# Optimization experiments

Hardware: AMD Instinct MI355X
Metric: run time of the kernel (lower is better)

The kernel has to match this reference:

```python
import jax, jax.numpy as jnp
import numpy as np

B, N, L, H, N_NODE, STEP = 512, 50, 50, 128, 100000, 1


def setup_inputs() -> dict:
    key = jax.random.key(0)
    ks = jax.random.split(key, 24)
    stdv = 1.0 / np.sqrt(H)
    u = lambda k, shape: jax.random.uniform(k, shape, jnp.float32, -stdv, stdv)
    inp = {
        "items": jax.random.randint(ks[0], (B, N), 0, N_NODE),
        "A": jax.random.uniform(ks[1], (B, N, 2 * N), jnp.float32),
        "alias_inputs": jax.random.randint(ks[2], (B, L), 0, N),
        "embedding": u(ks[3], (N_NODE, H)),
        "w_ih": u(ks[4], (3 * H, 2 * H)),
        "w_hh": u(ks[5], (3 * H, H)),
        "b_ih": u(ks[6], (3 * H,)),
        "b_hh": u(ks[7], (3 * H,)),
        "b_iah": u(ks[8], (H,)),
        "b_oah": u(ks[9], (H,)),
        "W_ein": u(ks[10], (H, H)), "b_ein": u(ks[11], (H,)),
        "W_eout": u(ks[12], (H, H)), "b_eout": u(ks[13], (H,)),
        "W1": u(ks[14], (H, H)), "b1": u(ks[15], (H,)),
        "W2": u(ks[16], (H, H)), "b2": u(ks[17], (H,)),
        "W3": u(ks[18], (1, H)),
        "Wt": u(ks[19], (H, 2 * H)), "bt": u(ks[20], (H,)),
    }
    return inp


def reference(items, A, alias_inputs, embedding, w_ih, w_hh, b_ih, b_hh,
              b_iah, b_oah, W_ein, b_ein, W_eout, b_eout,
              W1, b1, W2, b2, W3, Wt, bt):
    hidden = embedding[items]  # [B,N,H]
    A_in, A_out = A[:, :, :N], A[:, :, N:2 * N]
    for _ in range(STEP):
        # GRU-style GNN cell
        h_in = jnp.matmul(A_in, hidden @ W_ein.T + b_ein) + b_iah   # [B,N,H]
        h_out = jnp.matmul(A_out, hidden @ W_eout.T + b_eout) + b_oah
        inputs = jnp.concatenate([h_in, h_out], axis=2)             # [B,N,2H]
        gi = inputs @ w_ih.T + b_ih                                  # [B,N,3H]
        gh = hidden @ w_hh.T + b_hh
        i_r, i_i, i_n = jnp.split(gi, 3, axis=2)
        h_r, h_i, h_n = jnp.split(gh, 3, axis=2)
        resetgate = jax.nn.sigmoid(i_r + h_r)
        inputgate = jax.nn.sigmoid(i_i + h_i)
        newgate = jnp.tanh(i_n + resetgate * h_n)
        hidden = newgate + inputgate * (hidden - newgate)
    # gather per-position node states: seq_hidden[b, l] = hidden[b, alias[b, l]]
    mask = alias_inputs > 0  # [B,L]
    idx = jnp.broadcast_to(alias_inputs[:, :, None], (B, L, H))
    seq_hidden = jnp.take_along_axis(hidden, idx, axis=1)  # [B,L,H]
    last = jnp.sum(mask, axis=1) - 1
    ht = seq_hidden[jnp.arange(B), last]  # [B,H]
    # attention pooling
    q1 = (ht @ W1.T + b1)[:, None, :]      # [B,1,H]
    q2 = seq_hidden @ W2.T + b2            # [B,L,H]
    alpha = jax.nn.sigmoid(q1 + q2) @ W3.T  # [B,L,1]
    a = jnp.sum(alpha * seq_hidden * mask[:, :, None].astype(seq_hidden.dtype), axis=1)
    a = jnp.concatenate([a, ht], axis=1) @ Wt.T + bt  # [B,H]
    scores = a @ embedding[1:].T  # [B, n_node-1]
    return scores
```

## Files before the change

### kernel.cpp

```cpp
#include <hip/hip_runtime.h>

#define NB   512
#define NN   50
#define LLn  50
#define HD   128
#define OUTN 99999

#define WS_W1T   0
#define WS_W2T   65536
#define WS_WTT   131072
#define WS_WEH   262144
#define WS_WEL   327680
#define WS_WCATH 393216
#define WS_WCATL 688128
#define WS_AHI   983040
#define WS_ALO   1114112
#define WS_W2H   1245184
#define WS_W2L   1277952


typedef __attribute__((ext_vector_type(8))) short bf16x8;
typedef __attribute__((ext_vector_type(4))) float f32x4;

__device__ __forceinline__ unsigned short f2bf(float f) {
  unsigned int u = __float_as_uint(f);
  unsigned int r = (u + 0x7FFFu + ((u >> 16) & 1u)) >> 16;
  return (unsigned short)r;
}
__device__ __forceinline__ float bf2f(unsigned short h) {
  return __uint_as_float(((unsigned int)h) << 16);
}
__device__ __forceinline__ void cvt4(float4 v, ushort4& hi, ushort4& lo) {
  unsigned short h0 = f2bf(v.x), h1 = f2bf(v.y), h2 = f2bf(v.z), h3 = f2bf(v.w);
  hi = make_ushort4(h0, h1, h2, h3);
  lo = make_ushort4(f2bf(v.x - bf2f(h0)), f2bf(v.y - bf2f(h1)),
                    f2bf(v.z - bf2f(h2)), f2bf(v.w - bf2f(h3)));
}
__device__ __forceinline__ void gl_lds16(const void* g, void* l) {
  __builtin_amdgcn_global_load_lds(
      (const __attribute__((address_space(1))) void*)g,
      (__attribute__((address_space(3))) void*)l, 16, 0, 0);
}
__device__ __forceinline__ float sigm(float x) { return 1.f/(1.f + __expf(-x)); }

__global__ void k0_prep(const float* __restrict__ w_ih, const float* __restrict__ w_hh,
                        const float* __restrict__ W_ein, const float* __restrict__ W_eout,
                        const float* __restrict__ W1, const float* __restrict__ W2,
                        const float* __restrict__ Wt, char* __restrict__ wsb)
{
  float* wsf = (float*)wsb;
  for (int i = blockIdx.x * blockDim.x + threadIdx.x; i < 262144; i += gridDim.x * blockDim.x) {
    int idx = i;
    if (idx < 16384) { int k = idx >> 7, c = idx & 127; wsf[idx] = W1[c*128 + k]; continue; }
    idx -= 16384;
    if (idx < 16384) { int k = idx >> 7, c = idx & 127; wsf[16384 + idx] = W2[c*128 + k]; continue; }
    idx -= 16384;
    if (idx < 32768) { int k = idx >> 7, c = idx & 127; wsf[32768 + idx] = Wt[c*256 + k]; continue; }
    idx -= 32768;
    if (idx < 32768) {
      int n = idx >> 7, k = idx & 127;
      float v = (n < 128) ? W_ein[n*128 + k] : W_eout[(n-128)*128 + k];
      unsigned short h = f2bf(v);
      *(unsigned short*)(wsb + WS_WEH + idx*2) = h;
      *(unsigned short*)(wsb + WS_WEL + idx*2) = f2bf(v - bf2f(h));
      continue;
    }
    idx -= 32768;
    if (idx < 147456) {
      int n = idx / 384, k = idx % 384;
      float v = (k < 256) ? w_ih[n*256 + k] : w_hh[n*128 + (k - 256)];
      unsigned short h = f2bf(v);
      *(unsigned short*)(wsb + WS_WCATH + idx*2) = h;
      *(unsigned short*)(wsb + WS_WCATL + idx*2) = f2bf(v - bf2f(h));
      continue;
    }
    idx -= 147456;
    {
      float v = W2[idx];
      unsigned short h = f2bf(v);
      *(unsigned short*)(wsb + WS_W2H + idx*2) = h;
      *(unsigned short*)(wsb + WS_W2L + idx*2) = f2bf(v - bf2f(h));
    }
  }
}

__global__ __launch_bounds__(512) void k1f(const int* __restrict__ items,
    const float* __restrict__ A, const float* __restrict__ emb,
    const int* __restrict__ alias_in,
    const float* __restrict__ b_ein, const float* __restrict__ b_eout,
    const float* __restrict__ b_iah, const float* __restrict__ b_oah,
    const float* __restrict__ b_ih, const float* __restrict__ b_hh,
    const float* __restrict__ b1, const float* __restrict__ b2,
    const float* __restrict__ W3, const float* __restrict__ bt_,
    char* __restrict__ wsb)
{
  extern __shared__ char lds[];
  char*  IMG0H = lds;
  char*  IMG0L = lds + 16384;
  float* SIG   = (float*)lds;
  char*  HH    = lds + 32768;
  char*  HL    = lds + 49152;
  char*  HETH  = lds + 65536;
  char*  HETL  = lds + 98304;
  char*  IMG1H = lds + 65536;
  char*  IMG1L = lds + 81920;
  char*  H2H   = lds + 65536;
  char*  H2L   = lds + 81920;
  float* H2f   = (float*)(lds + 98304);
  float* Q1P   = (float*)(lds + 32768);
  float* AP    = (float*)(lds + 34816);
  float* RP    = (float*)(lds + 36864);
  float* ALP   = (float*)(lds + 38912);
  int*   ALI   = (int*)(lds + 39168);

  const int b = blockIdx.x, tid = threadIdx.x;
  const int lane = tid & 63, wid = tid >> 6, l15 = lane & 15, lq = lane >> 4;

  for (int i = tid; i < 7168; i += 512) {
    int bufsel = (i >= 3584), e = bufsel ? i - 3584 : i;
    int cc = e / 14, m = 50 + e % 14;
    unsigned adr = (unsigned)(cc*128) + (((unsigned)(m*2)) ^ (((unsigned)(cc&7)) << 4));
    *(unsigned short*)((bufsel ? HETL : HETH) + adr) = 0;
  }
  {
    const float* Ab = A + (size_t)b*NN*100;
    for (int i = tid; i < 8192; i += 512) {
      int sel = i >> 12, e = i & 4095, n = e >> 6, m = e & 63;
      float v = (n < 50 && m < 50) ? Ab[n*100 + sel*50 + m] : 0.f;
      unsigned short hi = f2bf(v);
      unsigned short lo = f2bf(v - bf2f(hi));
      unsigned adr = (unsigned)(n*128) + (((unsigned)(m*2)) ^ (((unsigned)(n&7)) << 4));
      *(unsigned short*)(lds + sel*16384 + adr) = hi;
      *(unsigned short*)(lds + sel*16384 + 8192 + adr) = lo;
    }
  }
  for (int i = tid; i < 2048; i += 512) {
    int row = i >> 5, part = i & 31;
    float4 v = make_float4(0.f,0.f,0.f,0.f);
    if (row < 50) {
      int it = items[b*NN + row];
      v = *(const float4*)&emb[(size_t)it*128 + part*4];
    }
    ushort4 h4v, g4v;
    cvt4(v, h4v, g4v);
    unsigned off = row*256 + (((unsigned)(part*8)) ^ (((unsigned)(row&7)) << 4));
    *(ushort4*)(HH + off) = h4v;
    *(ushort4*)(HL + off) = g4v;
  }
  __syncthreads();

  {
    f32x4 acc2[4][2];
#pragma unroll
    for (int i = 0; i < 4; ++i) { acc2[i][0] = (f32x4){0,0,0,0}; acc2[i][1] = (f32x4){0,0,0,0}; }
#pragma unroll
    for (int s = 0; s < 4; ++s) {
      bf16x8 ah[4], al[4];
#pragma unroll
      for (int i = 0; i < 4; ++i) {
        int row = i*16 + l15;
        unsigned off = row*256 + (((unsigned)(s*64 + lq*16)) ^ (((unsigned)(row&7)) << 4));
        ah[i] = *(const bf16x8*)(HH + off);
        al[i] = *(const bf16x8*)(HL + off);
      }
#pragma unroll
      for (int j = 0; j < 2; ++j) {
        int nc = wid*32 + j*16 + l15;
        unsigned boff = (unsigned)(nc*256 + s*64 + lq*16);
        bf16x8 bh = *(const bf16x8*)(wsb + WS_WEH + boff);
        bf16x8 bl = *(const bf16x8*)(wsb + WS_WEL + boff);
#pragma unroll
        for (int i = 0; i < 4; ++i) {
          acc2[i][j] = __builtin_amdgcn_mfma_f32_16x16x32_bf16(ah[i], bh, acc2[i][j], 0,0,0);
          acc2[i][j] = __builtin_amdgcn_mfma_f32_16x16x32_bf16(ah[i], bl, acc2[i][j], 0,0,0);
          acc2[i][j] = __builtin_amdgcn_mfma_f32_16x16x32_bf16(al[i], bh, acc2[i][j], 0,0,0);
        }
      }
    }
#pragma unroll
    for (int j = 0; j < 2; ++j) {
      int nc = wid*32 + j*16 + l15;
      float bv = (nc < 128) ? b_ein[nc] : b_eout[nc - 128];
#pragma unroll
      for (int i = 0; i < 4; ++i)
#pragma unroll
        for (int q = 0; q < 4; ++q) {
          int m = i*16 + lq*4 + q;
          if (m < 50) {
            float v = acc2[i][j][q] + bv;
            unsigned short hi = f2bf(v);
            unsigned short lo = f2bf(v - bf2f(hi));
            unsigned adr = (unsigned)(nc*128) + (((unsigned)(m*2)) ^ (((unsigned)(nc&7)) << 4));
            *(unsigned short*)(HETH + adr) = hi;
            *(unsigned short*)(HETL + adr) = lo;
          }
        }
    }
  }
  __syncthreads();

  {
    const int c = wid*16 + l15;
    f32x4 accS[2][4];
#pragma unroll
    for (int sel = 0; sel < 2; ++sel)
#pragma unroll
      for (int i = 0; i < 4; ++i) accS[sel][i] = (f32x4){0,0,0,0};
#pragma unroll
    for (int sel = 0; sel < 2; ++sel) {
#pragma unroll
      for (int s2 = 0; s2 < 2; ++s2) {
        int ct = sel*128 + c;
        unsigned badr = (unsigned)(ct*128) + (((unsigned)(s2*64 + lq*16)) ^ (((unsigned)(ct&7)) << 4));
        bf16x8 bh = *(const bf16x8*)(HETH + badr);
        bf16x8 bl = *(const bf16x8*)(HETL + badr);
#pragma unroll
        for (int i = 0; i < 4; ++i) {
          int n = i*16 + l15;
          unsigned aadr = (unsigned)(n*128) + (((unsigned)(s2*64 + lq*16)) ^ (((unsigned)(n&7)) << 4));
          bf16x8 ah = *(const bf16x8*)(lds + sel*16384 + aadr);
          bf16x8 al = *(const bf16x8*)(lds + sel*16384 + 8192 + aadr);
          accS[sel][i] = __builtin_amdgcn_mfma_f32_16x16x32_bf16(ah, bh, accS[sel][i], 0,0,0);
          accS[sel][i] = __builtin_amdgcn_mfma_f32_16x16x32_bf16(ah, bl, accS[sel][i], 0,0,0);
          accS[sel][i] = __builtin_amdgcn_mfma_f32_16x16x32_bf16(al, bh, accS[sel][i], 0,0,0);
        }
      }
    }
    __syncthreads();
#pragma unroll
    for (int sel = 0; sel < 2; ++sel) {
      float bv = sel ? b_oah[c] : b_iah[c];
      char* dH = sel ? IMG1H : IMG0H;
      char* dL = sel ? IMG1L : IMG0L;
#pragma unroll
      for (int i = 0; i < 4; ++i)
#pragma unroll
        for (int q = 0; q < 4; ++q) {
          int row = i*16 + lq*4 + q;
          float v = accS[sel][i][q] + bv;
          unsigned short hi = f2bf(v);
          unsigned short lo = f2bf(v - bf2f(hi));
          unsigned adr = row*256 + (((unsigned)(c*2)) ^ (((unsigned)(row&7)) << 4));
          *(unsigned short*)(dH + adr) = hi;
          *(unsigned short*)(dL + adr) = lo;
        }
    }
  }
  __syncthreads();

  f32x4 accRI[4][2], accNi[4], accNh[4];
#pragma unroll
  for (int i = 0; i < 4; ++i) {
    accRI[i][0] = (f32x4){0,0,0,0}; accRI[i][1] = (f32x4){0,0,0,0};
    accNi[i] = (f32x4){0,0,0,0};    accNh[i] = (f32x4){0,0,0,0};
  }
  const int nl = wid*16 + l15;

  auto cat_gemm = [&](const char* AH, const char* AL, int kh, bool toNh) {
#pragma unroll
    for (int s = 0; s < 4; ++s) {
      bf16x8 ah[4], al[4];
#pragma unroll
      for (int i = 0; i < 4; ++i) {
        int row = i*16 + l15;
        unsigned off = row*256 + (((unsigned)(s*64 + lq*16)) ^ (((unsigned)(row&7)) << 4));
        ah[i] = *(const bf16x8*)(AH + off);
        al[i] = *(const bf16x8*)(AL + off);
      }
#pragma unroll
      for (int g = 0; g < 2; ++g) {
        unsigned boff = (unsigned)((g*128 + nl)*768 + kh*256 + s*64 + lq*16);
        bf16x8 bh = *(const bf16x8*)(wsb + WS_WCATH + boff);
        bf16x8 bl = *(const bf16x8*)(wsb + WS_WCATL + boff);
#pragma unroll
        for (int i = 0; i < 4; ++i) {
          accRI[i][g] = __builtin_amdgcn_mfma_f32_16x16x32_bf16(ah[i], bh, accRI[i][g], 0,0,0);
          accRI[i][g] = __builtin_amdgcn_mfma_f32_16x16x32_bf16(ah[i], bl, accRI[i][g], 0,0,0);
          accRI[i][g] = __builtin_amdgcn_mfma_f32_16x16x32_bf16(al[i], bh, accRI[i][g], 0,0,0);
        }
      }
      {
        unsigned boff = (unsigned)((256 + nl)*768 + kh*256 + s*64 + lq*16);
        bf16x8 bh = *(const bf16x8*)(wsb + WS_WCATH + boff);
        bf16x8 bl = *(const bf16x8*)(wsb + WS_WCATL + boff);
        if (toNh) {
#pragma unroll
          for (int i = 0; i < 4; ++i) {
            accNh[i] = __builtin_amdgcn_mfma_f32_16x16x32_bf16(ah[i], bh, accNh[i], 0,0,0);
            accNh[i] = __builtin_amdgcn_mfma_f32_16x16x32_bf16(ah[i], bl, accNh[i], 0,0,0);
            accNh[i] = __builtin_amdgcn_mfma_f32_16x16x32_bf16(al[i], bh, accNh[i], 0,0,0);
          }
        } else {
#pragma unroll
          for (int i = 0; i < 4; ++i) {
            accNi[i] = __builtin_amdgcn_mfma_f32_16x16x32_bf16(ah[i], bh, accNi[i], 0,0,0);
            accNi[i] = __builtin_amdgcn_mfma_f32_16x16x32_bf16(ah[i], bl, accNi[i], 0,0,0);
            accNi[i] = __builtin_amdgcn_mfma_f32_16x16x32_bf16(al[i], bh, accNi[i], 0,0,0);
          }
        }
      }
    }
  };

  cat_gemm(IMG0H, IMG0L, 0, false);
  cat_gemm(IMG1H, IMG1L, 1, false);
  cat_gemm(HH,    HL,    2, true);
  __syncthreads();

  {
    const int c = nl;
    float bir = b_ih[c], bii = b_ih[128+c], bin_ = b_ih[256+c];
    float bhr = b_hh[c], bhi = b_hh[128+c], bhn  = b_hh[256+c];
#pragma unroll
    for (int i = 0; i < 4; ++i) {
#pragma unroll
      for (int q = 0; q < 4; ++q) {
        int row = i*16 + lq*4 + q;
        if (row < 50) {
          float rg = sigm(accRI[i][0][q] + bir + bhr);
          float ig = sigm(accRI[i][1][q] + bii + bhi);
          float ng_ = tanhf(accNi[i][q] + bin_ + rg*(accNh[i][q] + bhn));
          unsigned byte = row*256 + (((unsigned)(c*2)) ^ (((unsigned)(row&7)) << 4));
          float h = bf2f(*(const unsigned short*)(HH + byte))
                  + bf2f(*(const unsigned short*)(HL + byte));
          float hn = ng_ + ig*(h - ng_);
          H2f[row*128 + c] = hn;
          unsigned short hi = f2bf(hn);
          unsigned short lo = f2bf(hn - bf2f(hi));
          *(unsigned short*)(H2H + byte) = hi;
          *(unsigned short*)(H2L + byte) = lo;
        }
      }
    }
  }
  __syncthreads();

  if (tid < 64) ALI[tid] = (tid < LLn) ? alias_in[b*LLn + tid] : 0;
  __syncthreads();

  int cnt = 0;
  for (int l = 0; l < LLn; ++l) cnt += (ALI[l] > 0) ? 1 : 0;
  int last = cnt - 1; if (last < 0) last = LLn - 1;
  const int a_last = ALI[last];

  const int c = tid & 127, h4 = tid >> 7;
  const float* W1T = (const float*)(wsb + WS_W1T);
  const float* WtT = (const float*)(wsb + WS_WTT);

  {
    float q = 0.f;
    for (int k = h4*32; k < h4*32 + 32; k += 4) {
      float4 x = *(const float4*)&H2f[a_last*128 + k];
      q += x.x*W1T[(k<<7)+c] + x.y*W1T[((k+1)<<7)+c]
         + x.z*W1T[((k+2)<<7)+c] + x.w*W1T[((k+3)<<7)+c];
    }
    Q1P[h4*128 + c] = q;
  }
  __syncthreads();

  {
    const int cq = nl;
    f32x4 qa[4];
#pragma unroll
    for (int i = 0; i < 4; ++i) qa[i] = (f32x4){0,0,0,0};
#pragma unroll
    for (int s = 0; s < 4; ++s) {
      unsigned boff = (unsigned)(cq*256 + s*64 + lq*16);
      bf16x8 bh = *(const bf16x8*)(wsb + WS_W2H + boff);
      bf16x8 bl = *(const bf16x8*)(wsb + WS_W2L + boff);
#pragma unroll
      for (int i = 0; i < 4; ++i) {
        int ali = ALI[i*16 + l15];
        unsigned aadr = ali*256 + (((unsigned)(s*64 + lq*16)) ^ (((unsigned)(ali&7)) << 4));
        bf16x8 ah = *(const bf16x8*)(H2H + aadr);
        bf16x8 al = *(const bf16x8*)(H2L + aadr);
        qa[i] = __builtin_amdgcn_mfma_f32_16x16x32_bf16(ah, bh, qa[i], 0,0,0);
        qa[i] = __builtin_amdgcn_mfma_f32_16x16x32_bf16(ah, bl, qa[i], 0,0,0);
        qa[i] = __builtin_amdgcn_mfma_f32_16x16x32_bf16(al, bh, qa[i], 0,0,0);
      }
    }
    float q1c = Q1P[cq] + Q1P[128+cq] + Q1P[256+cq] + Q1P[384+cq] + b1[cq] + b2[cq];
#pragma unroll
    for (int i = 0; i < 4; ++i)
#pragma unroll
      for (int q = 0; q < 4; ++q) {
        int l = i*16 + lq*4 + q;
        if (l < 50) SIG[l*128 + cq] = sigm(q1c + qa[i][q]);
      }
  }
  __syncthreads();

  if (tid < 400) {
    int l = tid >> 3, qd = tid & 7;
    float sum = 0.f;
    for (int cc = qd*16; cc < qd*16 + 16; cc += 4) {
      float4 x = *(const float4*)&SIG[l*128 + cc];
      sum += x.x*W3[cc] + x.y*W3[cc+1] + x.z*W3[cc+2] + x.w*W3[cc+3];
    }
    sum += __shfl_xor(sum, 1);
    sum += __shfl_xor(sum, 2);
    sum += __shfl_xor(sum, 4);
    if (qd == 0) ALP[l] = (ALI[l] > 0) ? sum : 0.f;
  }
  __syncthreads();

  {
    float acc = 0.f;
    int l0 = h4*13, l1 = l0 + 13; if (l1 > LLn) l1 = LLn;
    for (int l = l0; l < l1; ++l)
      acc += ALP[l] * H2f[ALI[l]*128 + c];
    AP[h4*128 + c] = acc;
  }
  __syncthreads();

  {
    float r = 0.f;
    for (int k = h4*32; k < h4*32 + 32; ++k) {
      float av = AP[k] + AP[128+k] + AP[256+k] + AP[384+k];
      r += av * WtT[(k<<7) + c] + H2f[a_last*128 + k] * WtT[((128+k)<<7) + c];
    }
    RP[h4*128 + c] = r;
  }
  __syncthreads();

  if (tid < 128) {
    float r = bt_[c] + RP[c] + RP[128+c] + RP[256+c] + RP[384+c];
    int kh = c >> 6, kl = c & 63;
    unsigned int cb = (unsigned int)(kl*2) ^ (((unsigned int)(b & 7)) << 4);
    unsigned short hi = f2bf(r);
    unsigned short lo = f2bf(r - bf2f(hi));
    *(unsigned short*)(wsb + WS_AHI + kh*65536 + b*128 + cb) = hi;
    *(unsigned short*)(wsb + WS_ALO + kh*65536 + b*128 + cb) = lo;
  }
}

__global__ __launch_bounds__(512) void k2_mfma(const float* __restrict__ emb,
                                               const char* __restrict__ wsb,
                                               float* __restrict__ out)
{
  extern __shared__ char ldsc[];
  char* AHI = ldsc;
  char* ALO = ldsc + 32768;
  char* EHI = ldsc + 65536;
  char* ELO = ldsc + 81920;

  const int tid  = threadIdx.x;
  const int lane = tid & 63;
  const int wid  = tid >> 6;
  const int wm   = wid >> 1;
  const int wn   = wid & 1;
  const int j0   = blockIdx.x * 128;
  const int l15  = lane & 15, lq = lane >> 4;

  f32x4 acc[2][4][4];
#pragma unroll
  for (int bi = 0; bi < 2; ++bi)
#pragma unroll
    for (int i = 0; i < 4; ++i)
#pragma unroll
      for (int j = 0; j < 4; ++j) acc[bi][i][j] = (f32x4){0.f, 0.f, 0.f, 0.f};

  for (int kh = 0; kh < 2; ++kh) {
    {
      int rbase = tid >> 4, c4 = tid & 15;
#pragma unroll
      for (int rr = 0; rr < 4; ++rr) {
        int row = rbase + rr*32;
        int j = j0 + row; if (j > OUTN - 1) j = OUTN - 1;
        float4 v = *(const float4*)&emb[(size_t)(1 + j)*HD + kh*64 + c4*4];
        ushort4 hi4, lo4;
        cvt4(v, hi4, lo4);
        unsigned int off = (unsigned int)(row*128) + (((unsigned int)(c4*8)) ^ (((unsigned int)(row&7)) << 4));
        *(ushort4*)(EHI + off) = hi4;
        *(ushort4*)(ELO + off) = lo4;
      }
    }
#pragma unroll
    for (int bi = 0; bi < 2; ++bi) {
      const char* srcH = wsb + WS_AHI + kh*65536 + bi*32768;
      const char* srcL = wsb + WS_ALO + kh*65536 + bi*32768;
#pragma unroll
      for (int r = 0; r < 4; ++r) {
        int off = (r*512 + tid) * 16;
        gl_lds16(srcH + off, AHI + off);
        gl_lds16(srcL + off, ALO + off);
      }
      __syncthreads();

#pragma unroll
      for (int s = 0; s < 2; ++s) {
        bf16x8 ah[4], al[4], bh[4], bl[4];
        const unsigned int cb = (unsigned int)(s*64 + (lq << 4));
#pragma unroll
        for (int i = 0; i < 4; ++i) {
          int row = wm*64 + i*16 + l15;
          unsigned int off = (unsigned int)(row*128) + (cb ^ (((unsigned int)(row&7)) << 4));
          ah[i] = *(const bf16x8*)(AHI + off);
          al[i] = *(const bf16x8*)(ALO + off);
        }
#pragma unroll
        for (int j = 0; j < 4; ++j) {
          int row = wn*64 + j*16 + l15;
          unsigned int off = (unsigned int)(row*128) + (cb ^ (((unsigned int)(row&7)) << 4));
          bh[j] = *(const bf16x8*)(EHI + off);
          bl[j] = *(const bf16x8*)(ELO + off);
        }
#pragma unroll
        for (int i = 0; i < 4; ++i)
#pragma unroll
          for (int j = 0; j < 4; ++j) {
            acc[bi][i][j] = __builtin_amdgcn_mfma_f32_16x16x32_bf16(ah[i], bh[j], acc[bi][i][j], 0, 0, 0);
            acc[bi][i][j] = __builtin_amdgcn_mfma_f32_16x16x32_bf16(ah[i], bl[j], acc[bi][i][j], 0, 0, 0);
            acc[bi][i][j] = __builtin_amdgcn_mfma_f32_16x16x32_bf16(al[i], bh[j], acc[bi][i][j], 0, 0, 0);
          }
      }
      __syncthreads();
    }
  }

#pragma unroll
  for (int bi = 0; bi < 2; ++bi)
#pragma unroll
    for (int i = 0; i < 4; ++i) {
#pragma unroll
      for (int j = 0; j < 4; ++j) {
        int jj = j0 + wn*64 + j*16 + l15;
        if (jj < OUTN) {
          size_t rowbase = (size_t)(bi*256 + wm*64 + i*16 + lq*4);
#pragma unroll
          for (int q = 0; q < 4; ++q)
            out[(rowbase + q)*OUTN + jj] = acc[bi][i][j][q];
        }
      }
    }
}

extern "C" void kernel_launch(void* const* d_in, const int* in_sizes, int n_in,
                              void* d_out, int out_size, void* d_ws, size_t ws_size,
                              hipStream_t stream)
{
  const int*   items  = (const int*)  d_in[0];
  const float* A      = (const float*)d_in[1];
  const int*   alias  = (const int*)  d_in[2];
  const float* emb    = (const float*)d_in[3];
  const float* w_ih   = (const float*)d_in[4];
  const float* w_hh   = (const float*)d_in[5];
  const float* b_ih   = (const float*)d_in[6];
  const float* b_hh   = (const float*)d_in[7];
  const float* b_iah  = (const float*)d_in[8];
  const float* b_oah  = (const float*)d_in[9];
  const float* W_ein  = (const float*)d_in[10];
  const float* b_ein  = (const float*)d_in[11];
  const float* W_eout = (const float*)d_in[12];
  const float* b_eout = (const float*)d_in[13];
  const float* W1     = (const float*)d_in[14];
  const float* b1     = (const float*)d_in[15];
  const float* W2     = (const float*)d_in[16];
  const float* b2     = (const float*)d_in[17];
  const float* W3     = (const float*)d_in[18];
  const float* Wt     = (const float*)d_in[19];
  const float* bt_    = (const float*)d_in[20];

  char*  wsb  = (char*)d_ws;
  float* outf = (float*)d_out;

  k0_prep<<<240, 256, 0, stream>>>(w_ih, w_hh, W_ein, W_eout, W1, W2, Wt, wsb);

  k1f<<<NB, 512, 131072, stream>>>(items, A, emb, alias, b_ein, b_eout, b_iah, b_oah,
                                   b_ih, b_hh, b1, b2, W3, bt_, wsb);

  k2_mfma<<<dim3(782, 1), 512, 98304, stream>>>(emb, (const char*)d_ws, outf);
}
```

Baseline: 182.2 us.

## Shrink k1f to 256 threads with compact LDS and restructure k2 loop order

k1f now runs with 256 threads per block and about 78 KB of LDS instead of 512 threads and 128 KB, so two blocks can share a CU. To fit, the GNN phases are split into halves that reuse the same LDS buffers, with the A matrices restaged between phases. The fp32 hidden copy is dropped and values are rebuilt from the bf16 hi/lo pair. k2 now stages the whole embedding tile once into a doubled LDS region and loops over batch halves outermost, holding one accumulator set instead of two. This cuts register pressure but raises k2's LDS use, and k1f gains extra barriers and restaging work.

```diff
diff --git a/kernel.cpp b/kernel.cpp
--- a/kernel.cpp
+++ b/kernel.cpp
@@ -18,6 +18,18 @@
 #define WS_W2H   1245184
 #define WS_W2L   1277952
 
+#define LDS_HH    0
+#define LDS_HL    12800
+#define LDS_AIH   25600
+#define LDS_AIL   33792
+#define LDS_HETH  41984
+#define LDS_HETL  58368
+#define LDS_Q1P   74752
+#define LDS_AP    75776
+#define LDS_RP    76800
+#define LDS_ALP   77824
+#define LDS_ALI   78080
+#define K1F_LDS   78336
 
 typedef __attribute__((ext_vector_type(8))) short bf16x8;
 typedef __attribute__((ext_vector_type(4))) float f32x4;
@@ -84,7 +96,7 @@
   }
 }
 
-__global__ __launch_bounds__(512) void k1f(const int* __restrict__ items,
+__global__ __launch_bounds__(256, 2) void k1f(const int* __restrict__ items,
     const float* __restrict__ A, const float* __restrict__ emb,
     const int* __restrict__ alias_in,
     const float* __restrict__ b_ein, const float* __restrict__ b_eout,
@@ -95,99 +107,104 @@
     char* __restrict__ wsb)
 {
   extern __shared__ char lds[];
-  char*  IMG0H = lds;
-  char*  IMG0L = lds + 16384;
-  float* SIG   = (float*)lds;
-  char*  HH    = lds + 32768;
-  char*  HL    = lds + 49152;
-  char*  HETH  = lds + 65536;
-  char*  HETL  = lds + 98304;
-  char*  IMG1H = lds + 65536;
-  char*  IMG1L = lds + 81920;
-  char*  H2H   = lds + 65536;
-  char*  H2L   = lds + 81920;
-  float* H2f   = (float*)(lds + 98304);
-  float* Q1P   = (float*)(lds + 32768);
-  float* AP    = (float*)(lds + 34816);
-  float* RP    = (float*)(lds + 36864);
-  float* ALP   = (float*)(lds + 38912);
-  int*   ALI   = (int*)(lds + 39168);
+  char* HH   = lds + LDS_HH;
+  char* HL   = lds + LDS_HL;
+  char* AIH  = lds + LDS_AIH;
+  char* AIL  = lds + LDS_AIL;
+  char* HETH = lds + LDS_HETH;
+  char* HETL = lds + LDS_HETL;
+  char* H2H  = lds + 25600;
+  char* H2L  = lds + 38400;
+  float* SIG = (float*)lds;
+  float* Q1P = (float*)(lds + LDS_Q1P);
+  float* AP  = (float*)(lds + LDS_AP);
+  float* RP  = (float*)(lds + LDS_RP);
+  float* ALP = (float*)(lds + LDS_ALP);
+  int*   ALI = (int*)(lds + LDS_ALI);
 
   const int b = blockIdx.x, tid = threadIdx.x;
   const int lane = tid & 63, wid = tid >> 6, l15 = lane & 15, lq = lane >> 4;
-
-  for (int i = tid; i < 7168; i += 512) {
-    int bufsel = (i >= 3584), e = bufsel ? i - 3584 : i;
-    int cc = e / 14, m = 50 + e % 14;
-    unsigned adr = (unsigned)(cc*128) + (((unsigned)(m*2)) ^ (((unsigned)(cc&7)) << 4));
-    *(unsigned short*)((bufsel ? HETL : HETH) + adr) = 0;
-  }
-  {
-    const float* Ab = A + (size_t)b*NN*100;
-    for (int i = tid; i < 8192; i += 512) {
-      int sel = i >> 12, e = i & 4095, n = e >> 6, m = e & 63;
+  const float* Ab = A + (size_t)b*NN*100;
+
+  auto h2val = [&](int row, int k) -> float {
+    unsigned byte = (unsigned)(row*256) + (((unsigned)(k*2)) ^ (((unsigned)(row&7)) << 4));
+    return bf2f(*(const unsigned short*)(H2H + byte))
+         + bf2f(*(const unsigned short*)(H2L + byte));
+  };
+
+  auto stageA = [&](int sel) {
+    for (int i = tid; i < 4096; i += 256) {
+      int n = i >> 6, m = i & 63;
       float v = (n < 50 && m < 50) ? Ab[n*100 + sel*50 + m] : 0.f;
       unsigned short hi = f2bf(v);
       unsigned short lo = f2bf(v - bf2f(hi));
       unsigned adr = (unsigned)(n*128) + (((unsigned)(m*2)) ^ (((unsigned)(n&7)) << 4));
-      *(unsigned short*)(lds + sel*16384 + adr) = hi;
-      *(unsigned short*)(lds + sel*16384 + 8192 + adr) = lo;
-    }
-  }
-  for (int i = tid; i < 2048; i += 512) {
+      *(unsigned short*)(AIH + adr) = hi;
+      *(unsigned short*)(AIL + adr) = lo;
+    }
+  };
+
+  stageA(0);
+  for (int i = tid; i < 1600; i += 256) {
     int row = i >> 5, part = i & 31;
-    float4 v = make_float4(0.f,0.f,0.f,0.f);
-    if (row < 50) {
-      int it = items[b*NN + row];
-      v = *(const float4*)&emb[(size_t)it*128 + part*4];
-    }
+    int it = items[b*NN + row];
+    float4 v = *(const float4*)&emb[(size_t)it*128 + part*4];
     ushort4 h4v, g4v;
     cvt4(v, h4v, g4v);
     unsigned off = row*256 + (((unsigned)(part*8)) ^ (((unsigned)(row&7)) << 4));
     *(ushort4*)(HH + off) = h4v;
     *(ushort4*)(HL + off) = g4v;
   }
-  __syncthreads();
-
-  {
-    f32x4 acc2[4][2];
-#pragma unroll
-    for (int i = 0; i < 4; ++i) { acc2[i][0] = (f32x4){0,0,0,0}; acc2[i][1] = (f32x4){0,0,0,0}; }
+  if (tid < 64) ALI[tid] = (tid < LLn) ? alias_in[b*LLn + tid] : 0;
+  __syncthreads();
+
+  auto p2 = [&](int half) {
+    for (int i = tid; i < 3584; i += 256) {
+      int img = (i >= 1792), e = img ? i - 1792 : i;
+      int ct = e / 14, m = 50 + e % 14;
+      unsigned adr = (unsigned)(ct*128) + (((unsigned)(m*2)) ^ (((unsigned)(ct&7)) << 4));
+      *(unsigned short*)((img ? HETL : HETH) + adr) = 0;
+    }
+    f32x4 a2[2][4];
+#pragma unroll
+    for (int j = 0; j < 2; ++j)
+#pragma unroll
+      for (int i = 0; i < 4; ++i) a2[j][i] = (f32x4){0,0,0,0};
 #pragma unroll
     for (int s = 0; s < 4; ++s) {
-      bf16x8 ah[4], al[4];
+      bf16x8 ah[4], al4[4];
 #pragma unroll
       for (int i = 0; i < 4; ++i) {
         int row = i*16 + l15;
         unsigned off = row*256 + (((unsigned)(s*64 + lq*16)) ^ (((unsigned)(row&7)) << 4));
-        ah[i] = *(const bf16x8*)(HH + off);
-        al[i] = *(const bf16x8*)(HL + off);
+        ah[i]  = *(const bf16x8*)(HH + off);
+        al4[i] = *(const bf16x8*)(HL + off);
       }
 #pragma unroll
       for (int j = 0; j < 2; ++j) {
         int nc = wid*32 + j*16 + l15;
-        unsigned boff = (unsigned)(nc*256 + s*64 + lq*16);
+        unsigned boff = (unsigned)((half*128 + nc)*256 + s*64 + lq*16);
         bf16x8 bh = *(const bf16x8*)(wsb + WS_WEH + boff);
         bf16x8 bl = *(const bf16x8*)(wsb + WS_WEL + boff);
 #pragma unroll
         for (int i = 0; i < 4; ++i) {
-          acc2[i][j] = __builtin_amdgcn_mfma_f32_16x16x32_bf16(ah[i], bh, acc2[i][j], 0,0,0);
-          acc2[i][j] = __builtin_amdgcn_mfma_f32_16x16x32_bf16(ah[i], bl, acc2[i][j], 0,0,0);
-          acc2[i][j] = __builtin_amdgcn_mfma_f32_16x16x32_bf16(al[i], bh, acc2[i][j], 0,0,0);
+          a2[j][i] = __builtin_amdgcn_mfma_f32_16x16x32_bf16(ah[i], bh, a2[j][i], 0,0,0);
+          a2[j][i] = __builtin_amdgcn_mfma_f32_16x16x32_bf16(ah[i], bl, a2[j][i], 0,0,0);
+          a2[j][i] = __builtin_amdgcn_mfma_f32_16x16x32_bf16(al4[i], bh, a2[j][i], 0,0,0);
         }
       }
     }
 #pragma unroll
     for (int j = 0; j < 2; ++j) {
       int nc = wid*32 + j*16 + l15;
-      float bv = (nc < 128) ? b_ein[nc] : b_eout[nc - 128];
+      float bv = half ? b_eout[nc] : b_ein[nc];
 #pragma unroll
       for (int i = 0; i < 4; ++i)
 #pragma unroll
         for (int q = 0; q < 4; ++q) {
           int m = i*16 + lq*4 + q;
           if (m < 50) {
-            float v = acc2[i][j][q] + bv;
+            float v = a2[j][i][q] + bv;
             unsigned short hi = f2bf(v);
             unsigned short lo = f2bf(v - bf2f(hi));
             unsigned adr = (unsigned)(nc*128) + (((unsigned)(m*2)) ^ (((unsigned)(nc&7)) << 4));
@@ -196,146 +213,131 @@
           }
         }
     }
-  }
+  };
+
+  auto p3 = [&](int sel, int ctb, bool restage) {
+    f32x4 acc[4];
+#pragma unroll
+    for (int i = 0; i < 4; ++i) acc[i] = (f32x4){0,0,0,0};
+    const int ct = ctb*64 + wid*16 + l15;
+#pragma unroll
+    for (int s2 = 0; s2 < 2; ++s2) {
+      unsigned badr = (unsigned)(ct*128) + (((unsigned)(s2*64 + lq*16)) ^ (((unsigned)(ct&7)) << 4));
+      bf16x8 bh = *(const bf16x8*)(HETH + badr);
+      bf16x8 bl = *(const bf16x8*)(HETL + badr);
+#pragma unroll
+      for (int i = 0; i < 4; ++i) {
+        int n = i*16 + l15;
+        unsigned aadr = (unsigned)(n*128) + (((unsigned)(s2*64 + lq*16)) ^ (((unsigned)(n&7)) << 4));
+        bf16x8 ah  = *(const bf16x8*)(AIH + aadr);
+        bf16x8 al4 = *(const bf16x8*)(AIL + aadr);
+        acc[i] = __builtin_amdgcn_mfma_f32_16x16x32_bf16(ah, bh, acc[i], 0,0,0);
+        acc[i] = __builtin_amdgcn_mfma_f32_16x16x32_bf16(ah, bl, acc[i], 0,0,0);
+        acc[i] = __builtin_amdgcn_mfma_f32_16x16x32_bf16(al4, bh, acc[i], 0,0,0);
+      }
+    }
+    __syncthreads();
+    if (restage) stageA(1);
+    int cb = ctb*64 + wid*16 + l15;
+    float bv = sel ? b_oah[cb] : b_iah[cb];
+    char* dH = HETH + ctb*8192;
+    char* dL = HETL + ctb*8192;
+    int cw = wid*16 + l15;
+#pragma unroll
+    for (int i = 0; i < 4; ++i)
+#pragma unroll
+      for (int q = 0; q < 4; ++q) {
+        int row = i*16 + lq*4 + q;
+        float v = acc[i][q] + bv;
+        unsigned short hi = f2bf(v);
+        unsigned short lo = f2bf(v - bf2f(hi));
+        unsigned adr = (unsigned)(row*128) + (((unsigned)(cw*2)) ^ (((unsigned)(row&7)) << 4));
+        *(unsigned short*)(dH + adr) = hi;
+        *(unsigned short*)(dL + adr) = lo;
+      }
+  };
+
+  f32x4 accR[2][4], accI[2][4], accNi[2][4], accNh[2][4];
+#pragma unroll
+  for (int j2 = 0; j2 < 2; ++j2)
+#pragma unroll
+    for (int i = 0; i < 4; ++i) {
+      accR[j2][i] = (f32x4){0,0,0,0}; accI[j2][i] = (f32x4){0,0,0,0};
+      accNi[j2][i] = (f32x4){0,0,0,0}; accNh[j2][i] = (f32x4){0,0,0,0};
+    }
+
+  auto p4 = [&](const char* AH, const char* AL, int stride, int kbyte, int nS, bool toNh) {
+#pragma unroll
+    for (int s = 0; s < 4; ++s) {
+      if (s >= nS) break;
+      bf16x8 ah[4], al4[4];
+#pragma unroll
+      for (int i = 0; i < 4; ++i) {
+        int row = i*16 + l15;
+        unsigned off = (unsigned)(row*stride) + (((unsigned)(s*64 + lq*16)) ^ (((unsigned)(row&7)) << 4));
+        ah[i]  = *(const bf16x8*)(AH + off);
+        al4[i] = *(const bf16x8*)(AL + off);
+      }
+#pragma unroll
+      for (int g = 0; g < 3; ++g)
+#pragma unroll
+        for (int j2 = 0; j2 < 2; ++j2) {
+          int n = g*128 + wid*32 + j2*16 + l15;
+          unsigned boff = (unsigned)(n*768 + kbyte + s*64 + lq*16);
+          bf16x8 bh = *(const bf16x8*)(wsb + WS_WCATH + boff);
+          bf16x8 bl = *(const bf16x8*)(wsb + WS_WCATL + boff);
+          f32x4* tgt = (g == 0) ? accR[j2] : (g == 1) ? accI[j2] : (toNh ? accNh[j2] : accNi[j2]);
+#pragma unroll
+          for (int i = 0; i < 4; ++i) {
+            tgt[i] = __builtin_amdgcn_mfma_f32_16x16x32_bf16(ah[i], bh, tgt[i], 0,0,0);
+            tgt[i] = __builtin_amdgcn_mfma_f32_16x16x32_bf16(ah[i], bl, tgt[i], 0,0,0);
+            tgt[i] = __builtin_amdgcn_mfma_f32_16x16x32_bf16(al4[i], bh, tgt[i], 0,0,0);
+          }
+        }
+    }
+  };
+
+  p2(0);                    __syncthreads();
+  p3(0, 0, false);          __syncthreads();
+  p4(HETH, HETL, 128, 0, 2, false);
+  p3(0, 1, true);           __syncthreads();
+  p4(HETH + 8192, HETL + 8192, 128, 128, 2, false);
+  __syncthreads();
+  p2(1);                    __syncthreads();
+  p3(1, 0, false);          __syncthreads();
+  p4(HETH, HETL, 128, 256, 2, false);
+  p3(1, 1, false);          __syncthreads();
+  p4(HETH + 8192, HETL + 8192, 128, 384, 2, false);
+  p4(HH, HL, 256, 512, 4, true);
   __syncthreads();
 
   {
-    const int c = wid*16 + l15;
-    f32x4 accS[2][4];
-#pragma unroll
-    for (int sel = 0; sel < 2; ++sel)
-#pragma unroll
-      for (int i = 0; i < 4; ++i) accS[sel][i] = (f32x4){0,0,0,0};
-#pragma unroll
-    for (int sel = 0; sel < 2; ++sel) {
-#pragma unroll
-      for (int s2 = 0; s2 < 2; ++s2) {
-        int ct = sel*128 + c;
-        unsigned badr = (unsigned)(ct*128) + (((unsigned)(s2*64 + lq*16)) ^ (((unsigned)(ct&7)) << 4));
-        bf16x8 bh = *(const bf16x8*)(HETH + badr);
-        bf16x8 bl = *(const bf16x8*)(HETL + badr);
-#pragma unroll
-        for (int i = 0; i < 4; ++i) {
-          int n = i*16 + l15;
-          unsigned aadr = (unsigned)(n*128) + (((unsigned)(s2*64 + lq*16)) ^ (((unsigned)(n&7)) << 4));
-          bf16x8 ah = *(const bf16x8*)(lds + sel*16384 + aadr);
-          bf16x8 al = *(const bf16x8*)(lds + sel*16384 + 8192 + aadr);
-          accS[sel][i] = __builtin_amdgcn_mfma_f32_16x16x32_bf16(ah, bh, accS[sel][i], 0,0,0);
-          accS[sel][i] = __builtin_amdgcn_mfma_f32_16x16x32_bf16(ah, bl, accS[sel][i], 0,0,0);
-          accS[sel][i] = __builtin_amdgcn_mfma_f32_16x16x32_bf16(al, bh, accS[sel][i], 0,0,0);
-        }
-      }
-    }
-    __syncthreads();
-#pragma unroll
-    for (int sel = 0; sel < 2; ++sel) {
-      float bv = sel ? b_oah[c] : b_iah[c];
-      char* dH = sel ? IMG1H : IMG0H;
-      char* dL = sel ? IMG1L : IMG0L;
+#pragma unroll
+    for (int j2 = 0; j2 < 2; ++j2) {
+      int c = wid*32 + j2*16 + l15;
+      float bir = b_ih[c], bii = b_ih[128+c], bin_ = b_ih[256+c];
+      float bhr = b_hh[c], bhi = b_hh[128+c], bhn  = b_hh[256+c];
 #pragma unroll
       for (int i = 0; i < 4; ++i)
 #pragma unroll
         for (int q = 0; q < 4; ++q) {
           int row = i*16 + lq*4 + q;
-          float v = accS[sel][i][q] + bv;
-          unsigned short hi = f2bf(v);
-          unsigned short lo = f2bf(v - bf2f(hi));
-          unsigned adr = row*256 + (((unsigned)(c*2)) ^ (((unsigned)(row&7)) << 4));
-          *(unsigned short*)(dH + adr) = hi;
-          *(unsigned short*)(dL + adr) = lo;
-        }
-    }
-  }
-  __syncthreads();
-
-  f32x4 accRI[4][2], accNi[4], accNh[4];
-#pragma unroll
-  for (int i = 0; i < 4; ++i) {
-    accRI[i][0] = (f32x4){0,0,0,0}; accRI[i][1] = (f32x4){0,0,0,0};
-    accNi[i] = (f32x4){0,0,0,0};    accNh[i] = (f32x4){0,0,0,0};
-  }
-  const int nl = wid*16 + l15;
-
-  auto cat_gemm = [&](const char* AH, const char* AL, int kh, bool toNh) {
-#pragma unroll
-    for (int s = 0; s < 4; ++s) {
-      bf16x8 ah[4], al[4];
-#pragma unroll
-      for (int i = 0; i < 4; ++i) {
-        int row = i*16 + l15;
-        unsigned off = row*256 + (((unsigned)(s*64 + lq*16)) ^ (((unsigned)(row&7)) << 4));
-        ah[i] = *(const bf16x8*)(AH + off);
-        al[i] = *(const bf16x8*)(AL + off);
-      }
-#pragma unroll
-      for (int g = 0; g < 2; ++g) {
-        unsigned boff = (unsigned)((g*128 + nl)*768 + kh*256 + s*64 + lq*16);
-        bf16x8 bh = *(const bf16x8*)(wsb + WS_WCATH + boff);
-        bf16x8 bl = *(const bf16x8*)(wsb + WS_WCATL + boff);
-#pragma unroll
-        for (int i = 0; i < 4; ++i) {
-          accRI[i][g] = __builtin_amdgcn_mfma_f32_16x16x32_bf16(ah[i], bh, accRI[i][g], 0,0,0);
-          accRI[i][g] = __builtin_amdgcn_mfma_f32_16x16x32_bf16(ah[i], bl, accRI[i][g], 0,0,0);
-          accRI[i][g] = __builtin_amdgcn_mfma_f32_16x16x32_bf16(al[i], bh, accRI[i][g], 0,0,0);
-        }
-      }
-      {
-        unsigned boff = (unsigned)((256 + nl)*768 + kh*256 + s*64 + lq*16);
-        bf16x8 bh = *(const bf16x8*)(wsb + WS_WCATH + boff);
-        bf16x8 bl = *(const bf16x8*)(wsb + WS_WCATL + boff);
-        if (toNh) {
-#pragma unroll
-          for (int i = 0; i < 4; ++i) {
-            accNh[i] = __builtin_amdgcn_mfma_f32_16x16x32_bf16(ah[i], bh, accNh[i], 0,0,0);
-            accNh[i] = __builtin_amdgcn_mfma_f32_16x16x32_bf16(ah[i], bl, accNh[i], 0,0,0);
-            accNh[i] = __builtin_amdgcn_mfma_f32_16x16x32_bf16(al[i], bh, accNh[i], 0,0,0);
+          if (row < 50) {
+            float rg = sigm(accR[j2][i][q] + bir + bhr);
+            float ig = sigm(accI[j2][i][q] + bii + bhi);
+            float ng_ = tanhf(accNi[j2][i][q] + bin_ + rg*(accNh[j2][i][q] + bhn));
+            unsigned byte = (unsigned)(row*256) + (((unsigned)(c*2)) ^ (((unsigned)(row&7)) << 4));
+            float h = bf2f(*(const unsigned short*)(HH + byte))
+                    + bf2f(*(const unsigned short*)(HL + byte));
+            float hn = ng_ + ig*(h - ng_);
+            unsigned short hi = f2bf(hn);
+            unsigned short lo = f2bf(hn - bf2f(hi));
+            *(unsigned short*)(H2H + byte) = hi;
+            *(unsigned short*)(H2L + byte) = lo;
           }
-        } else {
-#pragma unroll
-          for (int i = 0; i < 4; ++i) {
-            accNi[i] = __builtin_amdgcn_mfma_f32_16x16x32_bf16(ah[i], bh, accNi[i], 0,0,0);
-            accNi[i] = __builtin_amdgcn_mfma_f32_16x16x32_bf16(ah[i], bl, accNi[i], 0,0,0);
-            accNi[i] = __builtin_amdgcn_mfma_f32_16x16x32_bf16(al[i], bh, accNi[i], 0,0,0);
-          }
-        }
-      }
-    }
-  };
-
-  cat_gemm(IMG0H, IMG0L, 0, false);
-  cat_gemm(IMG1H, IMG1L, 1, false);
-  cat_gemm(HH,    HL,    2, true);
-  __syncthreads();
-
-  {
-    const int c = nl;
-    float bir = b_ih[c], bii = b_ih[128+c], bin_ = b_ih[256+c];
-    float bhr = b_hh[c], bhi = b_hh[128+c], bhn  = b_hh[256+c];
-#pragma unroll
-    for (int i = 0; i < 4; ++i) {
-#pragma unroll
-      for (int q = 0; q < 4; ++q) {
-        int row = i*16 + lq*4 + q;
-        if (row < 50) {
-          float rg = sigm(accRI[i][0][q] + bir + bhr);
-          float ig = sigm(accRI[i][1][q] + bii + bhi);
-          float ng_ = tanhf(accNi[i][q] + bin_ + rg*(accNh[i][q] + bhn));
-          unsigned byte = row*256 + (((unsigned)(c*2)) ^ (((unsigned)(row&7)) << 4));
-          float h = bf2f(*(const unsigned short*)(HH + byte))
-                  + bf2f(*(const unsigned short*)(HL + byte));
-          float hn = ng_ + ig*(h - ng_);
-          H2f[row*128 + c] = hn;
-          unsigned short hi = f2bf(hn);
-          unsigned short lo = f2bf(hn - bf2f(hi));
-          *(unsigned short*)(H2H + byte) = hi;
-          *(unsigned short*)(H2L + byte) = lo;
-        }
-      }
-    }
-  }
-  __syncthreads();
-
-  if (tid < 64) ALI[tid] = (tid < LLn) ? alias_in[b*LLn + tid] : 0;
+        }
+    }
+  }
   __syncthreads();
 
   int cnt = 0;
@@ -343,88 +345,98 @@
   int last = cnt - 1; if (last < 0) last = LLn - 1;
   const int a_last = ALI[last];
 
-  const int c = tid & 127, h4 = tid >> 7;
+  const int c = tid & 127, h2 = tid >> 7;
   const float* W1T = (const float*)(wsb + WS_W1T);
   const float* WtT = (const float*)(wsb + WS_WTT);
 
   {
     float q = 0.f;
-    for (int k = h4*32; k < h4*32 + 32; k += 4) {
-      float4 x = *(const float4*)&H2f[a_last*128 + k];
-      q += x.x*W1T[(k<<7)+c] + x.y*W1T[((k+1)<<7)+c]
-         + x.z*W1T[((k+2)<<7)+c] + x.w*W1T[((k+3)<<7)+c];
-    }
-    Q1P[h4*128 + c] = q;
+    for (int k = h2*64; k < h2*64 + 64; ++k)
+      q += h2val(a_last, k) * W1T[(k<<7) + c];
+    Q1P[h2*128 + c] = q;
   }
   __syncthreads();
 
   {
-    const int cq = nl;
-    f32x4 qa[4];
-#pragma unroll
-    for (int i = 0; i < 4; ++i) qa[i] = (f32x4){0,0,0,0};
+    f32x4 qa[2][4];
+#pragma unroll
+    for (int j = 0; j < 2; ++j)
+#pragma unroll
+      for (int i = 0; i < 4; ++i) qa[j][i] = (f32x4){0,0,0,0};
 #pragma unroll
     for (int s = 0; s < 4; ++s) {
-      unsigned boff = (unsigned)(cq*256 + s*64 + lq*16);
-      bf16x8 bh = *(const bf16x8*)(wsb + WS_W2H + boff);
-      bf16x8 bl = *(const bf16x8*)(wsb + WS_W2L + boff);
+      bf16x8 ah[4], al4[4];
 #pragma unroll
       for (int i = 0; i < 4; ++i) {
         int ali = ALI[i*16 + l15];
-        unsigned aadr = ali*256 + (((unsigned)(s*64 + lq*16)) ^ (((unsigned)(ali&7)) << 4));
-        bf16x8 ah = *(const bf16x8*)(H2H + aadr);
-        bf16x8 al = *(const bf16x8*)(H2L + aadr);
-        qa[i] = __builtin_amdgcn_mfma_f32_16x16x32_bf16(ah, bh, qa[i], 0,0,0);
-        qa[i] = __builtin_amdgcn_mfma_f32_16x16x32_bf16(ah, bl, qa[i], 0,0,0);
-        qa[i] = __builtin_amdgcn_mfma_f32_16x16x32_bf16(al, bh, qa[i], 0,0,0);
-      }
-    }
-    float q1c = Q1P[cq] + Q1P[128+cq] + Q1P[256+cq] + Q1P[384+cq] + b1[cq] + b2[cq];
-#pragma unroll
-    for (int i = 0; i < 4; ++i)
-#pragma unroll
-      for (int q = 0; q < 4; ++q) {
-        int l = i*16 + lq*4 + q;
-        if (l < 50) SIG[l*128 + cq] = sigm(q1c + qa[i][q]);
-      }
-  }
-  __syncthreads();
-
-  if (tid < 400) {
-    int l = tid >> 3, qd = tid & 7;
+        unsigned aadr = (unsigned)(ali*256) + (((unsigned)(s*64 + lq*16)) ^ (((unsigned)(ali&7)) << 4));
+        ah[i]  = *(const bf16x8*)(H2H + aadr);
+        al4[i] = *(const bf16x8*)(H2L + aadr);
+      }
+#pragma unroll
+      for (int j = 0; j < 2; ++j) {
+        int cq = wid*32 + j*16 + l15;
+        unsigned boff = (unsigned)(cq*256 + s*64 + lq*16);
+        bf16x8 bh = *(const bf16x8*)(wsb + WS_W2H + boff);
+        bf16x8 bl = *(const bf16x8*)(wsb + WS_W2L + boff);
+#pragma unroll
+        for (int i = 0; i < 4; ++i) {
+          qa[j][i] = __builtin_amdgcn_mfma_f32_16x16x32_bf16(ah[i], bh, qa[j][i], 0,0,0);
+          qa[j][i] = __builtin_amdgcn_mfma_f32_16x16x32_bf16(ah[i], bl, qa[j][i], 0,0,0);
+          qa[j][i] = __builtin_amdgcn_mfma_f32_16x16x32_bf16(al4[i], bh, qa[j][i], 0,0,0);
+        }
+      }
+    }
+    __syncthreads();
+#pragma unroll
+    for (int j = 0; j < 2; ++j) {
+      int cq = wid*32 + j*16 + l15;
+      float q1c = Q1P[cq] + Q1P[128+cq] + b1[cq] + b2[cq];
+#pragma unroll
+      for (int i = 0; i < 4; ++i)
+#pragma unroll
+        for (int q = 0; q < 4; ++q) {
+          int l = i*16 + lq*4 + q;
+          if (l < 50) SIG[l*128 + cq] = sigm(q1c + qa[j][i][q]);
+        }
+    }
+  }
+  __syncthreads();
+
+  if (tid < 200) {
+    int l = tid >> 2, qd = tid & 3;
     float sum = 0.f;
-    for (int cc = qd*16; cc < qd*16 + 16; cc += 4) {
+    for (int cc = qd*32; cc < qd*32 + 32; cc += 4) {
       float4 x = *(const float4*)&SIG[l*128 + cc];
       sum += x.x*W3[cc] + x.y*W3[cc+1] + x.z*W3[cc+2] + x.w*W3[cc+3];
     }
     sum += __shfl_xor(sum, 1);
     sum += __shfl_xor(sum, 2);
-    sum += __shfl_xor(sum, 4);
     if (qd == 0) ALP[l] = (ALI[l] > 0) ? sum : 0.f;
   }
   __syncthreads();
 
   {
     float acc = 0.f;
-    int l0 = h4*13, l1 = l0 + 13; if (l1 > LLn) l1 = LLn;
-    for (int l = l0; l < l1; ++l)
-      acc += ALP[l] * H2f[ALI[l]*128 + c];
-    AP[h4*128 + c] = acc;
+    int l0 = h2*25;
+    for (int l = l0; l < l0 + 25; ++l)
+      acc += ALP[l] * h2val(ALI[l], c);
+    AP[h2*128 + c] = acc;
   }
   __syncthreads();
 
   {
     float r = 0.f;
-    for (int k = h4*32; k < h4*32 + 32; ++k) {
-      float av = AP[k] + AP[128+k] + AP[256+k] + AP[384+k];
-      r += av * WtT[(k<<7) + c] + H2f[a_last*128 + k] * WtT[((128+k)<<7) + c];
-    }
-    RP[h4*128 + c] = r;
+    for (int k = h2*64; k < h2*64 + 64; ++k) {
+      float av = AP[k] + AP[128+k];
+      r += av * WtT[(k<<7) + c] + h2val(a_last, k) * WtT[((128+k)<<7) + c];
+    }
+    RP[h2*128 + c] = r;
   }
   __syncthreads();
 
   if (tid < 128) {
-    float r = bt_[c] + RP[c] + RP[128+c] + RP[256+c] + RP[384+c];
+    float r = bt_[c] + RP[c] + RP[128+c];
     int kh = c >> 6, kl = c & 63;
     unsigned int cb = (unsigned int)(kl*2) ^ (((unsigned int)(b & 7)) << 4);
     unsigned short hi = f2bf(r);
@@ -441,8 +453,10 @@
   extern __shared__ char ldsc[];
   char* AHI = ldsc;
   char* ALO = ldsc + 32768;
-  char* EHI = ldsc + 65536;
-  char* ELO = ldsc + 81920;
+  char* EH0 = ldsc + 65536;
+  char* EL0 = ldsc + 81920;
+  char* EH1 = ldsc + 98304;
+  char* EL1 = ldsc + 114688;
 
   const int tid  = threadIdx.x;
   const int lane = tid & 63;
@@ -452,31 +466,28 @@
   const int j0   = blockIdx.x * 128;
   const int l15  = lane & 15, lq = lane >> 4;
 
-  f32x4 acc[2][4][4];
-#pragma unroll
-  for (int bi = 0; bi < 2; ++bi)
+  for (int e = tid; e < 4096; e += 512) {
+    int row = e >> 5, c4 = e & 31;
+    int j = j0 + row; if (j > OUTN - 1) j = OUTN - 1;
+    float4 v = *(const float4*)&emb[(size_t)(1 + j)*HD + c4*4];
+    ushort4 hi4, lo4;
+    cvt4(v, hi4, lo4);
+    int kh = c4 >> 4, cc = c4 & 15;
+    unsigned off = (unsigned)(row*128) + (((unsigned)(cc*8)) ^ (((unsigned)(row&7)) << 4));
+    *(ushort4*)((kh ? EH1 : EH0) + off) = hi4;
+    *(ushort4*)((kh ? EL1 : EL0) + off) = lo4;
+  }
+
+#pragma unroll
+  for (int bi = 0; bi < 2; ++bi) {
+    f32x4 acc[4][4];
 #pragma unroll
     for (int i = 0; i < 4; ++i)
 #pragma unroll
-      for (int j = 0; j < 4; ++j) acc[bi][i][j] = (f32x4){0.f, 0.f, 0.f, 0.f};
-
-  for (int kh = 0; kh < 2; ++kh) {
-    {
-      int rbase = tid >> 4, c4 = tid & 15;
-#pragma unroll
-      for (int rr = 0; rr < 4; ++rr) {
-        int row = rbase + rr*32;
-        int j = j0 + row; if (j > OUTN - 1) j = OUTN - 1;
-        float4 v = *(const float4*)&emb[(size_t)(1 + j)*HD + kh*64 + c4*4];
-        ushort4 hi4, lo4;
-        cvt4(v, hi4, lo4);
-        unsigned int off = (unsigned int)(row*128) + (((unsigned int)(c4*8)) ^ (((unsigned int)(row&7)) << 4));
-        *(ushort4*)(EHI + off) = hi4;
-        *(ushort4*)(ELO + off) = lo4;
-      }
-    }
-#pragma unroll
-    for (int bi = 0; bi < 2; ++bi) {
+      for (int j = 0; j < 4; ++j) acc[i][j] = (f32x4){0.f, 0.f, 0.f, 0.f};
+
+#pragma unroll
+    for (int kh = 0; kh < 2; ++kh) {
       const char* srcH = wsb + WS_AHI + kh*65536 + bi*32768;
       const char* srcL = wsb + WS_ALO + kh*65536 + bi*32768;
 #pragma unroll
@@ -486,6 +497,8 @@
         gl_lds16(srcL + off, ALO + off);
       }
       __syncthreads();
+      const char* EHI = kh ? EH1 : EH0;
+      const char* ELO = kh ? EL1 : EL0;
 
 #pragma unroll
       for (int s = 0; s < 2; ++s) {
@@ -509,17 +522,14 @@
         for (int i = 0; i < 4; ++i)
 #pragma unroll
           for (int j = 0; j < 4; ++j) {
-            acc[bi][i][j] = __builtin_amdgcn_mfma_f32_16x16x32_bf16(ah[i], bh[j], acc[bi][i][j], 0, 0, 0);
-            acc[bi][i][j] = __builtin_amdgcn_mfma_f32_16x16x32_bf16(ah[i], bl[j], acc[bi][i][j], 0, 0, 0);
-            acc[bi][i][j] = __builtin_amdgcn_mfma_f32_16x16x32_bf16(al[i], bh[j], acc[bi][i][j], 0, 0, 0);
+            acc[i][j] = __builtin_amdgcn_mfma_f32_16x16x32_bf16(ah[i], bh[j], acc[i][j], 0, 0, 0);
+            acc[i][j] = __builtin_amdgcn_mfma_f32_16x16x32_bf16(ah[i], bl[j], acc[i][j], 0, 0, 0);
+            acc[i][j] = __builtin_amdgcn_mfma_f32_16x16x32_bf16(al[i], bh[j], acc[i][j], 0, 0, 0);
           }
       }
       __syncthreads();
     }
-  }
-
-#pragma unroll
-  for (int bi = 0; bi < 2; ++bi)
+
 #pragma unroll
     for (int i = 0; i < 4; ++i) {
 #pragma unroll
@@ -529,10 +539,11 @@
           size_t rowbase = (size_t)(bi*256 + wm*64 + i*16 + lq*4);
 #pragma unroll
           for (int q = 0; q < 4; ++q)
-            out[(rowbase + q)*OUTN + jj] = acc[bi][i][j][q];
-        }
-      }
-    }
+            out[(rowbase + q)*OUTN + jj] = acc[i][j][q];
+        }
+      }
+    }
+  }
 }
 
 extern "C" void kernel_launch(void* const* d_in, const int* in_sizes, int n_in,
@@ -566,8 +577,8 @@
 
   k0_prep<<<240, 256, 0, stream>>>(w_ih, w_hh, W_ein, W_eout, W1, W2, Wt, wsb);
 
-  k1f<<<NB, 512, 131072, stream>>>(items, A, emb, alias, b_ein, b_eout, b_iah, b_oah,
-                                   b_ih, b_hh, b1, b2, W3, bt_, wsb);
-
-  k2_mfma<<<dim3(782, 1), 512, 98304, stream>>>(emb, (const char*)d_ws, outf);
-}
+  k1f<<<NB, 256, K1F_LDS, stream>>>(items, A, emb, alias, b_ein, b_eout, b_iah, b_oah,
+                                    b_ih, b_hh, b1, b2, W3, bt_, wsb);
+
+  k2_mfma<<<dim3(782, 1), 512, 131072, stream>>>(emb, (const char*)d_ws, outf);
+}
```

Measured after the change: 201.7 us. 1.11x slower.
